# Optimization experiments

Measured on AMD Instinct MI355X. Metric: run time of the kernel, lower is better.

The kernel has to match this reference:

```python
import jax, jax.numpy as jnp
import numpy as np

H = 128          # hidden_size
GRID = 4         # grid_dim
CELL = 0.5       # cell_size
PRED_LEN = 12
EMB = H // 4     # social pooling embed dim = 32


def setup_inputs() -> dict:
    key = jax.random.key(0)
    ks = jax.random.split(key, 13)
    B, N, T = 16384, 64, 8
    s = 0.05
    return {
        "obs": jax.random.normal(ks[0], (B, T, 2), jnp.float32),
        "neighbors": jax.random.normal(ks[1], (B, N, T, 2), jnp.float32),
        "embed_table": jax.random.normal(ks[2], (GRID * GRID + 1, EMB), jnp.float32) * s,
        "W_in": jax.random.normal(ks[3], (H, 2), jnp.float32) * s,
        "b_in": jax.random.normal(ks[4], (H,), jnp.float32) * s,
        "W_sp": jax.random.normal(ks[5], (H, EMB), jnp.float32) * s,
        "b_sp": jax.random.normal(ks[6], (H,), jnp.float32) * s,
        "W_ih": jax.random.normal(ks[7], (4 * H, 2 * H), jnp.float32) * s,
        "W_hh": jax.random.normal(ks[8], (4 * H, H), jnp.float32) * s,
        "b_ih": jax.random.normal(ks[9], (4 * H,), jnp.float32) * s,
        "b_hh": jax.random.normal(ks[10], (4 * H,), jnp.float32) * s,
        "W_out": jax.random.normal(ks[11], (2, H), jnp.float32) * s,
        "b_out": jax.random.normal(ks[12], (2,), jnp.float32) * s,
    }


def reference(obs, neighbors, embed_table, W_in, b_in, W_sp, b_sp,
              W_ih, W_hh, b_ih, b_hh, W_out, b_out):
    B = obs.shape[0]
    half = GRID // 2

    def pool(rel):  # rel: [B, N, 2] -> [B, EMB]
        idx = jnp.clip(jnp.floor(rel / CELL).astype(jnp.int32), -half, half - 1) + half
        # after clamp+shift, idx in [0, GRID-1], so index is always valid (matches torch path)
        flat = idx[..., 0] * GRID + idx[..., 1]  # [B, N]
        return embed_table[flat].sum(axis=1)     # sum-pool over neighbors

    def lstm(h, c, x):  # torch LSTMCell gate order: i, f, g, o
        gates = x @ W_ih.T + b_ih + h @ W_hh.T + b_hh  # [B, 4H]
        i, f, g, o = jnp.split(gates, 4, axis=-1)
        c2 = jax.nn.sigmoid(f) * c + jax.nn.sigmoid(i) * jnp.tanh(g)
        h2 = jax.nn.sigmoid(o) * jnp.tanh(c2)
        return h2, c2

    def obs_step(carry, xs):
        h, c = carry
        o_t, nb_t = xs  # [B,2], [B,N,2]
        agent = o_t @ W_in.T + b_in                        # [B,H]
        social = pool(nb_t - o_t[:, None, :]) @ W_sp.T + b_sp  # [B,H]
        h, c = lstm(h, c, jnp.concatenate([agent, social], axis=-1))
        return (h, c), None

    h0 = jnp.zeros((B, H), obs.dtype)
    c0 = jnp.zeros((B, H), obs.dtype)
    obs_tf = jnp.swapaxes(obs, 0, 1)          # [T,B,2]
    nb_tf = jnp.moveaxis(neighbors, 2, 0)     # [T,B,N,2]
    (h, c), _ = jax.lax.scan(obs_step, (h0, c0), (obs_tf, nb_tf))

    def pred_step(carry, _):
        h, c, prev = carry
        agent = prev @ W_in.T + b_in
        x = jnp.concatenate([agent, jnp.zeros_like(agent)], axis=-1)
        h, c = lstm(h, c, x)
        disp = h @ W_out.T + b_out  # [B,2]
        return (h, c, disp), disp

    prev0 = jnp.zeros((B, 2), obs.dtype)
    _, fut = jax.lax.scan(pred_step, (h, c, prev0), None, length=PRED_LEN)
    return jnp.swapaxes(fut, 0, 1)  # [B, PRED_LEN, 2]
```

## Files before the change

kernel.cpp:

```cpp
#include <hip/hip_runtime.h>
#include <math.h>

typedef _Float16 f16;
typedef f16 f16x8 __attribute__((ext_vector_type(8)));
typedef float f32x4 __attribute__((ext_vector_type(4)));

#define Bsz   16384
#define Tobs  8
#define PREDL 12
#define MR    32

__device__ __forceinline__ float fast_sigm(float x) {
  float e = __builtin_amdgcn_exp2f(-1.44269504f * x);
  return __builtin_amdgcn_rcpf(1.f + e);
}
__device__ __forceinline__ float fast_tanh(float x) {
  float e = __builtin_amdgcn_exp2f(2.88539008f * x);
  return 1.f - 2.f * __builtin_amdgcn_rcpf(1.f + e);
}


#define HB(buf, ct, kt, lane, j) (((((buf)*2 + (ct))*4 + (kt))*64 + (lane))*8 + (j))
#define CX(t, ct, lane, j) ((((t)*2 + (ct))*64 + (lane))*8 + (j))
#define WF(ktw, w, rt, lane) ((size_t)((((ktw)*16 + (w))*2 + (rt))*64 + (lane)) * 8)

__global__ __launch_bounds__(64) void pack_all(
    const float* __restrict__ W_ih, const float* __restrict__ W_hh,
    const float* __restrict__ W_in, const float* __restrict__ W_sp,
    const float* __restrict__ table,
    const float* __restrict__ b_in, const float* __restrict__ b_sp,
    const float* __restrict__ b_ih, const float* __restrict__ b_hh,
    const float* __restrict__ W_out, const float* __restrict__ b_out,
    f16* __restrict__ Wfrag, float* __restrict__ biasO,
    float* __restrict__ biasP, float* __restrict__ biasPE) {
  const int jo = blockIdx.x;
  const int g = jo >> 7, hc = jo & 127;
  const int w = hc >> 3, rt = (hc >> 2) & 1, qq = hc & 3;
  const int rowr = qq * 4 + g;
  const int m = threadIdx.x;
  __shared__ float wspPS[32];
  __shared__ float cellsS[16];

  float a0 = W_ih[jo * 256 + m],        a1 = W_ih[jo * 256 + 64 + m];
  float s0 = W_ih[jo * 256 + 128 + m],  s1 = W_ih[jo * 256 + 192 + m];
  float hh0 = W_hh[jo * 128 + m],       hh1 = W_hh[jo * 128 + 64 + m];
  float bi0 = b_in[m], bi1 = b_in[64 + m];
  float bs0 = b_sp[m], bs1 = b_sp[64 + m];
  float wi00 = W_in[m * 2 + 0],        wi01 = W_in[m * 2 + 1];
  float wi10 = W_in[(64 + m) * 2 + 0], wi11 = W_in[(64 + m) * 2 + 1];

  auto red = [](float v) {
#pragma unroll
    for (int s = 1; s < 64; s <<= 1) v += __shfl_xor(v, s);
    return v;
  };

#pragma unroll 4
  for (int e = 0; e < 32; ++e) {
    float wp = red(s0 * W_sp[m * 32 + e] + s1 * W_sp[(64 + m) * 32 + e]);
    if (m == e) wspPS[e] = wp;
  }
  __syncthreads();
  if (m < 16) {
    float s = 0.f;
#pragma unroll
    for (int e = 0; e < 32; ++e) s += table[m * 32 + e] * wspPS[e];
    cellsS[m] = s;
  }

  float wio0 = red(a0 * wi00 + a1 * wi10);
  float wio1 = red(a0 * wi01 + a1 * wi11);
  float dotA = red(a0 * bi0 + a1 * bi1);
  float dotS = red(s0 * bs0 + s1 * bs1);

  float eff0 = hh0 + wio0 * W_out[m]      + wio1 * W_out[128 + m];
  float eff1 = hh1 + wio0 * W_out[64 + m] + wio1 * W_out[192 + m];

  const int lane_w = ((m >> 3) & 3) * 16 + rowr;
  const int j_w = m & 7, kh = m >> 5;
  Wfrag[WF(kh,     w, rt, lane_w) + j_w] = (f16)hh0;
  Wfrag[WF(2 + kh, w, rt, lane_w) + j_w] = (f16)hh1;
  Wfrag[WF(5 + kh, w, rt, lane_w) + j_w] = (f16)eff0;
  Wfrag[WF(7 + kh, w, rt, lane_w) + j_w] = (f16)eff1;

  if (m < 32) {
    float x = (m < 16) ? cellsS[m] : (m == 16 ? wio0 : (m == 17 ? wio1 : 0.f));
    Wfrag[WF(4, w, rt, (m >> 3) * 16 + rowr) + (m & 7)] = (f16)x;
  }
  if (m == 36) {
    const int idx = ((w * 2 + rt) * 4 + qq) * 4 + g;
    const float base = b_ih[jo] + b_hh[jo];
    biasO[idx] = base + dotA + dotS;
    biasP[idx] = base + dotA;
    biasPE[idx] = base + dotA + wio0 * b_out[0] + wio1 * b_out[1];
  }
}

__global__ __launch_bounds__(1024, 4) void social_lstm_main(
    const float* __restrict__ obs, const float* __restrict__ nb,
    const f16* __restrict__ Wfrag, const float* __restrict__ biasO,
    const float* __restrict__ biasP, const float* __restrict__ biasPE,
    const float* __restrict__ W_out, const float* __restrict__ b_out,
    float* __restrict__ out) {
  __shared__ __align__(16) f16 Hbuf[2 * 2 * 4 * 64 * 8];
  __shared__ __align__(16) f16 cntX[8 * 2 * 64 * 8];

  const int tid = threadIdx.x;
  const int w = tid >> 6, ln = tid & 63;
  const int q = ln >> 4, c = ln & 15;
  const int b0 = blockIdx.x * MR;

  for (int i = tid; i < 2048; i += 1024) ((uint32_t*)Hbuf)[i] = 0u;
  for (int i = tid; i < 8192; i += 1024) ((uint32_t*)cntX)[i] = 0u;
  __syncthreads();

  {
    const int r = tid >> 5;
    const int lg = tid & 31;
    const float4* orow = (const float4*)(obs + (size_t)(b0 + r) * 16);
    float4 O0 = orow[0], O1 = orow[1], O2 = orow[2], O3 = orow[3];
    float ox[8] = {O0.x, O0.z, O1.x, O1.z, O2.x, O2.z, O3.x, O3.z};
    float oy[8] = {O0.y, O0.w, O1.y, O1.w, O2.y, O2.w, O3.y, O3.w};
    unsigned long long h[8] = {0ull, 0ull, 0ull, 0ull, 0ull, 0ull, 0ull, 0ull};
#pragma unroll
    for (int jt = 0; jt < 2; ++jt) {
      int trk = lg + 32 * jt;
      const float4* tr = (const float4*)(nb + ((size_t)(b0 + r) * 64 + trk) * 16);
      float4 T0 = tr[0], T1 = tr[1], T2 = tr[2], T3 = tr[3];
      float nx[8] = {T0.x, T0.z, T1.x, T1.z, T2.x, T2.z, T3.x, T3.z};
      float ny[8] = {T0.y, T0.w, T1.y, T1.w, T2.y, T2.w, T3.y, T3.w};
#pragma unroll
      for (int t = 0; t < 8; ++t) {
        float rx = nx[t] - ox[t], ry = ny[t] - oy[t];
        int ix = (int)floorf(rx + rx);
        int iy = (int)floorf(ry + ry);
        ix = min(max(ix, -2), 1);
        iy = min(max(iy, -2), 1);
        int flat = (ix + 2) * 4 + (iy + 2);
        h[t] += 1ull << (flat * 4);
      }
    }
    auto shx = [](unsigned long long x, int msk) {
      unsigned lo = __shfl_xor((unsigned)x, msk);
      unsigned hi = __shfl_xor((unsigned)(x >> 32), msk);
      return ((unsigned long long)hi << 32) | lo;
    };
#pragma unroll
    for (int t = 0; t < 8; ++t) {
      unsigned long long e0 = h[t] & 0x0F0F0F0F0F0F0F0Full;
      unsigned long long e1 = (h[t] >> 4) & 0x0F0F0F0F0F0F0F0Full;
      e0 += shx(e0, 1);  e1 += shx(e1, 1);
      e0 += shx(e0, 2);  e1 += shx(e1, 2);
      e0 += shx(e0, 4);  e1 += shx(e1, 4);
      e0 += shx(e0, 8);  e1 += shx(e1, 8);
      e0 += shx(e0, 16); e1 += shx(e1, 16);
      if (lg < 16) {
        unsigned long long src = (lg & 1) ? e1 : e0;
        unsigned cnt = (unsigned)(src >> ((lg >> 1) * 8)) & 0xFFu;
        cntX[CX(t, r >> 4, (lg >> 3) * 16 + (r & 15), lg & 7)] = (f16)(float)cnt;
      }
    }
    if (lg < 8) {
      float xv = obs[(size_t)(b0 + r) * 16 + lg * 2];
      float yv = obs[(size_t)(b0 + r) * 16 + lg * 2 + 1];
      cntX[CX(lg, r >> 4, 2 * 16 + (r & 15), 0)] = (f16)xv;
      cntX[CX(lg, r >> 4, 2 * 16 + (r & 15), 1)] = (f16)yv;
    }
  }

  f16x8 Wh[2][4];
#pragma unroll
  for (int rt = 0; rt < 2; ++rt)
#pragma unroll
    for (int kt = 0; kt < 4; ++kt)
      Wh[rt][kt] = *(const f16x8*)(Wfrag + WF(kt, w, rt, ln));

  float creg[4] = {0.f, 0.f, 0.f, 0.f};
  const int ktw_i = w >> 2;
  const int lnw = (w & 3) * 16 + c;
  const int bi0i = (w * 2 + 0) * 4 + q, bi1i = (w * 2 + 1) * 4 + q;

  auto epi = [&](f32x4 a, int rt, int ct, int wb) {
    float iv = fast_sigm(a[0]), fv = fast_sigm(a[1]);
    float gv = fast_tanh(a[2]), ov = fast_sigm(a[3]);
    int ci = rt * 2 + ct;
    float c2 = fv * creg[ci] + iv * gv;
    creg[ci] = c2;
    float hv = ov * fast_tanh(c2);
    Hbuf[HB(wb, ct, ktw_i, lnw, rt * 4 + q)] = (f16)hv;
  };

  auto hh_chain = [&](int rb, f32x4& a00, f32x4& a01, f32x4& a10, f32x4& a11) {
#pragma unroll
    for (int kt = 0; kt < 4; ++kt) {
      f16x8 h0 = *(const f16x8*)&Hbuf[HB(rb, 0, kt, ln, 0)];
      f16x8 h1 = *(const f16x8*)&Hbuf[HB(rb, 1, kt, ln, 0)];
      a00 = __builtin_amdgcn_mfma_f32_16x16x32_f16(Wh[0][kt], h0, a00, 0, 0, 0);
      a01 = __builtin_amdgcn_mfma_f32_16x16x32_f16(Wh[0][kt], h1, a01, 0, 0, 0);
      a10 = __builtin_amdgcn_mfma_f32_16x16x32_f16(Wh[1][kt], h0, a10, 0, 0, 0);
      a11 = __builtin_amdgcn_mfma_f32_16x16x32_f16(Wh[1][kt], h1, a11, 0, 0, 0);
    }
  };

  {
    f16x8 Bx0 = *(const f16x8*)(Wfrag + WF(4, w, 0, ln));
    f16x8 Bx1 = *(const f16x8*)(Wfrag + WF(4, w, 1, ln));
#pragma unroll
    for (int t = 0; t < Tobs; ++t) {
      const int rb = t & 1, wb = rb ^ 1;
      __syncthreads();
      float4 bv0 = ((const float4*)biasO)[bi0i];
      float4 bv1 = ((const float4*)biasO)[bi1i];
      f32x4 a00 = (f32x4){bv0.x, bv0.y, bv0.z, bv0.w}, a01 = a00;
      f32x4 a10 = (f32x4){bv1.x, bv1.y, bv1.z, bv1.w}, a11 = a10;
      f16x8 c0 = *(const f16x8*)&cntX[CX(t, 0, ln, 0)];
      f16x8 c1 = *(const f16x8*)&cntX[CX(t, 1, ln, 0)];
      a00 = __builtin_amdgcn_mfma_f32_16x16x32_f16(Bx0, c0, a00, 0, 0, 0);
      a01 = __builtin_amdgcn_mfma_f32_16x16x32_f16(Bx0, c1, a01, 0, 0, 0);
      a10 = __builtin_amdgcn_mfma_f32_16x16x32_f16(Bx1, c0, a10, 0, 0, 0);
      a11 = __builtin_amdgcn_mfma_f32_16x16x32_f16(Bx1, c1, a11, 0, 0, 0);
      hh_chain(rb, a00, a01, a10, a11);
      epi(a00, 0, 0, wb); epi(a01, 0, 1, wb);
      epi(a10, 1, 0, wb); epi(a11, 1, 1, wb);
    }
  }

  {
    const int rb = Tobs & 1, wb = rb ^ 1;
    __syncthreads();
    float4 bv0 = ((const float4*)biasP)[bi0i];
    float4 bv1 = ((const float4*)biasP)[bi1i];
    f32x4 a00 = (f32x4){bv0.x, bv0.y, bv0.z, bv0.w}, a01 = a00;
    f32x4 a10 = (f32x4){bv1.x, bv1.y, bv1.z, bv1.w}, a11 = a10;
    hh_chain(rb, a00, a01, a10, a11);
    epi(a00, 0, 0, wb); epi(a01, 0, 1, wb);
    epi(a10, 1, 0, wb); epi(a11, 1, 1, wb);
  }

#pragma unroll
  for (int rt = 0; rt < 2; ++rt)
#pragma unroll
    for (int kt = 0; kt < 4; ++kt)
      Wh[rt][kt] = *(const f16x8*)(Wfrag + WF(5 + kt, w, rt, ln));

  const int d_oi = tid >> 4, d_s = tid & 15;
  const int d_row = d_oi >> 1, d_jj = d_oi & 1;
  const float d_bo = b_out[d_jj];

  auto disp_out = [&](int rbuf, int p) {
    const float4* wp = (const float4*)(W_out + d_jj * 128 + d_s * 8);
    float4 w0 = wp[0], w1 = wp[1];
    f16x8 h8 = *(const f16x8*)&Hbuf[
        HB(rbuf, d_row >> 4, d_s >> 2, (d_s & 3) * 16 + (d_row & 15), 0)];
    float s = w0.x * (float)h8[0] + w0.y * (float)h8[1] +
              w0.z * (float)h8[2] + w0.w * (float)h8[3] +
              w1.x * (float)h8[4] + w1.y * (float)h8[5] +
              w1.z * (float)h8[6] + w1.w * (float)h8[7];
    s += __shfl_xor(s, 1);
    s += __shfl_xor(s, 2);
    s += __shfl_xor(s, 4);
    s += __shfl_xor(s, 8);
    if ((tid & 15) == 0)
      out[(size_t)(b0 + d_row) * (PREDL * 2) + p * 2 + d_jj] = s + d_bo;
  };

  for (int p = 1; p < PREDL; ++p) {
    const int st = Tobs + p;
    const int rb = st & 1, wb = rb ^ 1;
    __syncthreads();
    disp_out(rb, p - 1);
    float4 bv0 = ((const float4*)biasPE)[bi0i];
    float4 bv1 = ((const float4*)biasPE)[bi1i];
    f32x4 a00 = (f32x4){bv0.x, bv0.y, bv0.z, bv0.w}, a01 = a00;
    f32x4 a10 = (f32x4){bv1.x, bv1.y, bv1.z, bv1.w}, a11 = a10;
    hh_chain(rb, a00, a01, a10, a11);
    epi(a00, 0, 0, wb); epi(a01, 0, 1, wb);
    epi(a10, 1, 0, wb); epi(a11, 1, 1, wb);
  }
  __syncthreads();
  disp_out((Tobs + PREDL) & 1, PREDL - 1);
}

extern "C" void kernel_launch(void* const* d_in, const int* in_sizes, int n_in,
                              void* d_out, int out_size, void* d_ws, size_t ws_size,
                              hipStream_t stream) {
  const float* obs   = (const float*)d_in[0];
  const float* nbrs  = (const float*)d_in[1];
  const float* table = (const float*)d_in[2];
  const float* W_in  = (const float*)d_in[3];
  const float* b_in  = (const float*)d_in[4];
  const float* W_sp  = (const float*)d_in[5];
  const float* b_sp  = (const float*)d_in[6];
  const float* W_ih  = (const float*)d_in[7];
  const float* W_hh  = (const float*)d_in[8];
  const float* b_ih  = (const float*)d_in[9];
  const float* b_hh  = (const float*)d_in[10];
  const float* W_out = (const float*)d_in[11];
  const float* b_out = (const float*)d_in[12];
  float* out = (float*)d_out;

  char* ws = (char*)d_ws;
  f16*   Wfrag  = (f16*)(ws);
  float* biasO  = (float*)(ws + 294912);
  float* biasP  = (float*)(ws + 296960);
  float* biasPE = (float*)(ws + 299008);

  pack_all<<<512, 64, 0, stream>>>(W_ih, W_hh, W_in, W_sp, table, b_in, b_sp, b_ih, b_hh,
                                   W_out, b_out, Wfrag, biasO, biasP, biasPE);
  social_lstm_main<<<Bsz / MR, 1024, 0, stream>>>(obs, nbrs, Wfrag, biasO, biasP, biasPE,
                                                  W_out, b_out, out);
}
```

Baseline: 210.9 us.

## Process two 32-row groups per block with interleaved MFMA chains and packed h stores

Measured after the change: 205.1 us. 2.8% less time.

```diff
diff --git a/kernel.cpp b/kernel.cpp
--- a/kernel.cpp
+++ b/kernel.cpp
@@ -2,13 +2,14 @@
 #include <math.h>
 
 typedef _Float16 f16;
+typedef f16 f16x2 __attribute__((ext_vector_type(2)));
 typedef f16 f16x8 __attribute__((ext_vector_type(8)));
 typedef float f32x4 __attribute__((ext_vector_type(4)));
 
 #define Bsz   16384
 #define Tobs  8
 #define PREDL 12
-#define MR    32
+#define MR    64
 
 __device__ __forceinline__ float fast_sigm(float x) {
   float e = __builtin_amdgcn_exp2f(-1.44269504f * x);
@@ -20,8 +21,6 @@
 }
 
 
-#define HB(buf, ct, kt, lane, j) (((((buf)*2 + (ct))*4 + (kt))*64 + (lane))*8 + (j))
-#define CX(t, ct, lane, j) ((((t)*2 + (ct))*64 + (lane))*8 + (j))
 #define WF(ktw, w, rt, lane) ((size_t)((((ktw)*16 + (w))*2 + (rt))*64 + (lane)) * 8)
 
 __global__ __launch_bounds__(64) void pack_all(
@@ -32,7 +31,8 @@
     const float* __restrict__ b_ih, const float* __restrict__ b_hh,
     const float* __restrict__ W_out, const float* __restrict__ b_out,
     f16* __restrict__ Wfrag, float* __restrict__ biasO,
-    float* __restrict__ biasP, float* __restrict__ biasPE) {
+    float* __restrict__ biasP, float* __restrict__ biasPE,
+    float* __restrict__ W_outP) {
   const int jo = blockIdx.x;
   const int g = jo >> 7, hc = jo & 127;
   const int w = hc >> 3, rt = (hc >> 2) & 1, qq = hc & 3;
@@ -76,8 +76,9 @@
   float eff0 = hh0 + wio0 * W_out[m]      + wio1 * W_out[128 + m];
   float eff1 = hh1 + wio0 * W_out[64 + m] + wio1 * W_out[192 + m];
 
-  const int lane_w = ((m >> 3) & 3) * 16 + rowr;
-  const int j_w = m & 7, kh = m >> 5;
+  const int km = (m & 0x78) | (2 * (m & 3) + ((m >> 2) & 1));
+  const int lane_w = ((km >> 3) & 3) * 16 + rowr;
+  const int j_w = km & 7, kh = km >> 5;
   Wfrag[WF(kh,     w, rt, lane_w) + j_w] = (f16)hh0;
   Wfrag[WF(2 + kh, w, rt, lane_w) + j_w] = (f16)hh1;
   Wfrag[WF(5 + kh, w, rt, lane_w) + j_w] = (f16)eff0;
@@ -94,37 +95,47 @@
     biasP[idx] = base + dotA;
     biasPE[idx] = base + dotA + wio0 * b_out[0] + wio1 * b_out[1];
   }
-}
-
-__global__ __launch_bounds__(1024, 4) void social_lstm_main(
+  if (jo == 0) {
+    W_outP[km]            = W_out[m];
+    W_outP[km + 64]       = W_out[m + 64];
+    W_outP[128 + km]      = W_out[128 + m];
+    W_outP[128 + km + 64] = W_out[128 + m + 64];
+  }
+}
+
+__global__ __launch_bounds__(1024) void social_lstm_main(
     const float* __restrict__ obs, const float* __restrict__ nb,
     const f16* __restrict__ Wfrag, const float* __restrict__ biasO,
     const float* __restrict__ biasP, const float* __restrict__ biasPE,
-    const float* __restrict__ W_out, const float* __restrict__ b_out,
+    const float* __restrict__ W_outP, const float* __restrict__ b_out,
     float* __restrict__ out) {
-  __shared__ __align__(16) f16 Hbuf[2 * 2 * 4 * 64 * 8];
-  __shared__ __align__(16) f16 cntX[8 * 2 * 64 * 8];
+  __shared__ __align__(16) f16 Hbuf[2][2][2][4][64][8];
+  __shared__ __align__(16) f16 cntX[2][8][2][64][8];
 
   const int tid = threadIdx.x;
   const int w = tid >> 6, ln = tid & 63;
   const int q = ln >> 4, c = ln & 15;
+  const int whi = w >> 2, wlo = w & 3;
   const int b0 = blockIdx.x * MR;
 
-  for (int i = tid; i < 2048; i += 1024) ((uint32_t*)Hbuf)[i] = 0u;
-  for (int i = tid; i < 8192; i += 1024) ((uint32_t*)cntX)[i] = 0u;
+  for (int i = tid; i < 16384; i += 1024) {
+    ((uint32_t*)Hbuf)[i] = 0u;
+    ((uint32_t*)cntX)[i] = 0u;
+  }
   __syncthreads();
 
   {
-    const int r = tid >> 5;
-    const int lg = tid & 31;
+    const int r = tid >> 4;
+    const int lg = tid & 15;
+    const int pG = r >> 5, prr = r & 31;
     const float4* orow = (const float4*)(obs + (size_t)(b0 + r) * 16);
     float4 O0 = orow[0], O1 = orow[1], O2 = orow[2], O3 = orow[3];
     float ox[8] = {O0.x, O0.z, O1.x, O1.z, O2.x, O2.z, O3.x, O3.z};
     float oy[8] = {O0.y, O0.w, O1.y, O1.w, O2.y, O2.w, O3.y, O3.w};
     unsigned long long h[8] = {0ull, 0ull, 0ull, 0ull, 0ull, 0ull, 0ull, 0ull};
 #pragma unroll
-    for (int jt = 0; jt < 2; ++jt) {
-      int trk = lg + 32 * jt;
+    for (int jt = 0; jt < 4; ++jt) {
+      int trk = lg + 16 * jt;
       const float4* tr = (const float4*)(nb + ((size_t)(b0 + r) * 64 + trk) * 16);
       float4 T0 = tr[0], T1 = tr[1], T2 = tr[2], T3 = tr[3];
       float nx[8] = {T0.x, T0.z, T1.x, T1.z, T2.x, T2.z, T3.x, T3.z};
@@ -149,22 +160,19 @@
     for (int t = 0; t < 8; ++t) {
       unsigned long long e0 = h[t] & 0x0F0F0F0F0F0F0F0Full;
       unsigned long long e1 = (h[t] >> 4) & 0x0F0F0F0F0F0F0F0Full;
-      e0 += shx(e0, 1);  e1 += shx(e1, 1);
-      e0 += shx(e0, 2);  e1 += shx(e1, 2);
-      e0 += shx(e0, 4);  e1 += shx(e1, 4);
-      e0 += shx(e0, 8);  e1 += shx(e1, 8);
-      e0 += shx(e0, 16); e1 += shx(e1, 16);
-      if (lg < 16) {
-        unsigned long long src = (lg & 1) ? e1 : e0;
-        unsigned cnt = (unsigned)(src >> ((lg >> 1) * 8)) & 0xFFu;
-        cntX[CX(t, r >> 4, (lg >> 3) * 16 + (r & 15), lg & 7)] = (f16)(float)cnt;
-      }
+      e0 += shx(e0, 1); e1 += shx(e1, 1);
+      e0 += shx(e0, 2); e1 += shx(e1, 2);
+      e0 += shx(e0, 4); e1 += shx(e1, 4);
+      e0 += shx(e0, 8); e1 += shx(e1, 8);
+      unsigned long long src = (lg & 1) ? e1 : e0;
+      unsigned cnt = (unsigned)(src >> ((lg >> 1) * 8)) & 0xFFu;
+      cntX[pG][t][prr >> 4][(lg >> 3) * 16 + (prr & 15)][lg & 7] = (f16)(float)cnt;
     }
     if (lg < 8) {
       float xv = obs[(size_t)(b0 + r) * 16 + lg * 2];
       float yv = obs[(size_t)(b0 + r) * 16 + lg * 2 + 1];
-      cntX[CX(lg, r >> 4, 2 * 16 + (r & 15), 0)] = (f16)xv;
-      cntX[CX(lg, r >> 4, 2 * 16 + (r & 15), 1)] = (f16)yv;
+      cntX[pG][lg][prr >> 4][2 * 16 + (prr & 15)][0] = (f16)xv;
+      cntX[pG][lg][prr >> 4][2 * 16 + (prr & 15)][1] = (f16)yv;
     }
   }
 
@@ -175,107 +183,124 @@
     for (int kt = 0; kt < 4; ++kt)
       Wh[rt][kt] = *(const f16x8*)(Wfrag + WF(kt, w, rt, ln));
 
-  float creg[4] = {0.f, 0.f, 0.f, 0.f};
-  const int ktw_i = w >> 2;
-  const int lnw = (w & 3) * 16 + c;
-  const int bi0i = (w * 2 + 0) * 4 + q, bi1i = (w * 2 + 1) * 4 + q;
-
-  auto epi = [&](f32x4 a, int rt, int ct, int wb) {
+  float cr[8];
+#pragma unroll
+  for (int i = 0; i < 8; ++i) cr[i] = 0.f;
+
+  auto ldbias = [&](const float* bp, f32x4& v0, f32x4& v1) {
+    float4 t0 = ((const float4*)bp)[(w * 2 + 0) * 4 + q];
+    float4 t1 = ((const float4*)bp)[(w * 2 + 1) * 4 + q];
+    v0 = (f32x4){t0.x, t0.y, t0.z, t0.w};
+    v1 = (f32x4){t1.x, t1.y, t1.z, t1.w};
+  };
+
+  auto mf = [](f16x8 a, f16x8 b, f32x4 cc) {
+    return __builtin_amdgcn_mfma_f32_16x16x32_f16(a, b, cc, 0, 0, 0);
+  };
+
+  auto cell = [&](const f32x4& a, float& ccst) {
     float iv = fast_sigm(a[0]), fv = fast_sigm(a[1]);
     float gv = fast_tanh(a[2]), ov = fast_sigm(a[3]);
-    int ci = rt * 2 + ct;
-    float c2 = fv * creg[ci] + iv * gv;
-    creg[ci] = c2;
-    float hv = ov * fast_tanh(c2);
-    Hbuf[HB(wb, ct, ktw_i, lnw, rt * 4 + q)] = (f16)hv;
-  };
-
-  auto hh_chain = [&](int rb, f32x4& a00, f32x4& a01, f32x4& a10, f32x4& a11) {
+    ccst = fv * ccst + iv * gv;
+    return ov * fast_tanh(ccst);
+  };
+
+  f16x8 Bx0 = *(const f16x8*)(Wfrag + WF(4, w, 0, ln));
+  f16x8 Bx1 = *(const f16x8*)(Wfrag + WF(4, w, 1, ln));
+
+  f32x4 bv0, bv1;
+  ldbias(biasO, bv0, bv1);
+
+  auto step = [&](int rb, int wb, bool ex, int t) {
+    f32x4 A00 = bv0, A01 = bv0, A10 = bv1, A11 = bv1;
+    f32x4 B00 = bv0, B01 = bv0, B10 = bv1, B11 = bv1;
+    if (ex) {
+      f16x8 ca0 = *(const f16x8*)&cntX[0][t][0][ln][0];
+      f16x8 ca1 = *(const f16x8*)&cntX[0][t][1][ln][0];
+      A00 = mf(Bx0, ca0, A00); A01 = mf(Bx0, ca1, A01);
+      A10 = mf(Bx1, ca0, A10); A11 = mf(Bx1, ca1, A11);
+      f16x8 cb0 = *(const f16x8*)&cntX[1][t][0][ln][0];
+      f16x8 cb1 = *(const f16x8*)&cntX[1][t][1][ln][0];
+      B00 = mf(Bx0, cb0, B00); B01 = mf(Bx0, cb1, B01);
+      B10 = mf(Bx1, cb0, B10); B11 = mf(Bx1, cb1, B11);
+    }
 #pragma unroll
     for (int kt = 0; kt < 4; ++kt) {
-      f16x8 h0 = *(const f16x8*)&Hbuf[HB(rb, 0, kt, ln, 0)];
-      f16x8 h1 = *(const f16x8*)&Hbuf[HB(rb, 1, kt, ln, 0)];
-      a00 = __builtin_amdgcn_mfma_f32_16x16x32_f16(Wh[0][kt], h0, a00, 0, 0, 0);
-      a01 = __builtin_amdgcn_mfma_f32_16x16x32_f16(Wh[0][kt], h1, a01, 0, 0, 0);
-      a10 = __builtin_amdgcn_mfma_f32_16x16x32_f16(Wh[1][kt], h0, a10, 0, 0, 0);
-      a11 = __builtin_amdgcn_mfma_f32_16x16x32_f16(Wh[1][kt], h1, a11, 0, 0, 0);
-    }
-  };
-
-  {
-    f16x8 Bx0 = *(const f16x8*)(Wfrag + WF(4, w, 0, ln));
-    f16x8 Bx1 = *(const f16x8*)(Wfrag + WF(4, w, 1, ln));
-#pragma unroll
-    for (int t = 0; t < Tobs; ++t) {
-      const int rb = t & 1, wb = rb ^ 1;
-      __syncthreads();
-      float4 bv0 = ((const float4*)biasO)[bi0i];
-      float4 bv1 = ((const float4*)biasO)[bi1i];
-      f32x4 a00 = (f32x4){bv0.x, bv0.y, bv0.z, bv0.w}, a01 = a00;
-      f32x4 a10 = (f32x4){bv1.x, bv1.y, bv1.z, bv1.w}, a11 = a10;
-      f16x8 c0 = *(const f16x8*)&cntX[CX(t, 0, ln, 0)];
-      f16x8 c1 = *(const f16x8*)&cntX[CX(t, 1, ln, 0)];
-      a00 = __builtin_amdgcn_mfma_f32_16x16x32_f16(Bx0, c0, a00, 0, 0, 0);
-      a01 = __builtin_amdgcn_mfma_f32_16x16x32_f16(Bx0, c1, a01, 0, 0, 0);
-      a10 = __builtin_amdgcn_mfma_f32_16x16x32_f16(Bx1, c0, a10, 0, 0, 0);
-      a11 = __builtin_amdgcn_mfma_f32_16x16x32_f16(Bx1, c1, a11, 0, 0, 0);
-      hh_chain(rb, a00, a01, a10, a11);
-      epi(a00, 0, 0, wb); epi(a01, 0, 1, wb);
-      epi(a10, 1, 0, wb); epi(a11, 1, 1, wb);
-    }
-  }
-
-  {
-    const int rb = Tobs & 1, wb = rb ^ 1;
+      f16x8 h0 = *(const f16x8*)&Hbuf[0][rb][0][kt][ln][0];
+      f16x8 h1 = *(const f16x8*)&Hbuf[0][rb][1][kt][ln][0];
+      A00 = mf(Wh[0][kt], h0, A00); A01 = mf(Wh[0][kt], h1, A01);
+      A10 = mf(Wh[1][kt], h0, A10); A11 = mf(Wh[1][kt], h1, A11);
+    }
+#pragma unroll
+    for (int kt = 0; kt < 4; ++kt) {
+      f16x8 h0 = *(const f16x8*)&Hbuf[1][rb][0][kt][ln][0];
+      f16x8 h1 = *(const f16x8*)&Hbuf[1][rb][1][kt][ln][0];
+      B00 = mf(Wh[0][kt], h0, B00); B01 = mf(Wh[0][kt], h1, B01);
+      B10 = mf(Wh[1][kt], h0, B10); B11 = mf(Wh[1][kt], h1, B11);
+    }
+    {
+      f16x2 pk;
+      pk[0] = (f16)cell(A00, cr[0]); pk[1] = (f16)cell(A10, cr[2]);
+      *(f16x2*)&Hbuf[0][wb][0][whi][wlo * 16 + c][2 * q] = pk;
+      pk[0] = (f16)cell(A01, cr[1]); pk[1] = (f16)cell(A11, cr[3]);
+      *(f16x2*)&Hbuf[0][wb][1][whi][wlo * 16 + c][2 * q] = pk;
+      pk[0] = (f16)cell(B00, cr[4]); pk[1] = (f16)cell(B10, cr[6]);
+      *(f16x2*)&Hbuf[1][wb][0][whi][wlo * 16 + c][2 * q] = pk;
+      pk[0] = (f16)cell(B01, cr[5]); pk[1] = (f16)cell(B11, cr[7]);
+      *(f16x2*)&Hbuf[1][wb][1][whi][wlo * 16 + c][2 * q] = pk;
+    }
+  };
+
+#pragma unroll
+  for (int t = 0; t < Tobs; ++t) {
+    const int rb = t & 1;
     __syncthreads();
-    float4 bv0 = ((const float4*)biasP)[bi0i];
-    float4 bv1 = ((const float4*)biasP)[bi1i];
-    f32x4 a00 = (f32x4){bv0.x, bv0.y, bv0.z, bv0.w}, a01 = a00;
-    f32x4 a10 = (f32x4){bv1.x, bv1.y, bv1.z, bv1.w}, a11 = a10;
-    hh_chain(rb, a00, a01, a10, a11);
-    epi(a00, 0, 0, wb); epi(a01, 0, 1, wb);
-    epi(a10, 1, 0, wb); epi(a11, 1, 1, wb);
-  }
+    step(rb, rb ^ 1, true, t);
+  }
+
+  ldbias(biasP, bv0, bv1);
+  __syncthreads();
+  step(0, 1, false, 0);
 
 #pragma unroll
   for (int rt = 0; rt < 2; ++rt)
 #pragma unroll
     for (int kt = 0; kt < 4; ++kt)
       Wh[rt][kt] = *(const f16x8*)(Wfrag + WF(5 + kt, w, rt, ln));
-
-  const int d_oi = tid >> 4, d_s = tid & 15;
+  ldbias(biasPE, bv0, bv1);
+
+  const int d_oi = tid >> 3, d_s8 = tid & 7;
   const int d_row = d_oi >> 1, d_jj = d_oi & 1;
+  const int dG = d_row >> 5, drr = d_row & 31;
+  const int d_ct = drr >> 4, d_c = drr & 15;
+  const int d_kt = d_s8 >> 1, d_fl = (2 * (d_s8 & 1)) * 16 + d_c;
   const float d_bo = b_out[d_jj];
 
   auto disp_out = [&](int rbuf, int p) {
-    const float4* wp = (const float4*)(W_out + d_jj * 128 + d_s * 8);
-    float4 w0 = wp[0], w1 = wp[1];
-    f16x8 h8 = *(const f16x8*)&Hbuf[
-        HB(rbuf, d_row >> 4, d_s >> 2, (d_s & 3) * 16 + (d_row & 15), 0)];
-    float s = w0.x * (float)h8[0] + w0.y * (float)h8[1] +
-              w0.z * (float)h8[2] + w0.w * (float)h8[3] +
-              w1.x * (float)h8[4] + w1.y * (float)h8[5] +
-              w1.z * (float)h8[6] + w1.w * (float)h8[7];
+    const float4* wp = (const float4*)(W_outP + d_jj * 128 + d_s8 * 16);
+    float4 w0 = wp[0], w1 = wp[1], w2 = wp[2], w3 = wp[3];
+    f16x8 e0 = *(const f16x8*)&Hbuf[dG][rbuf][d_ct][d_kt][d_fl][0];
+    f16x8 e1 = *(const f16x8*)&Hbuf[dG][rbuf][d_ct][d_kt][d_fl + 16][0];
+    float s = w0.x * (float)e0[0] + w0.y * (float)e0[1] +
+              w0.z * (float)e0[2] + w0.w * (float)e0[3] +
+              w1.x * (float)e0[4] + w1.y * (float)e0[5] +
+              w1.z * (float)e0[6] + w1.w * (float)e0[7] +
+              w2.x * (float)e1[0] + w2.y * (float)e1[1] +
+              w2.z * (float)e1[2] + w2.w * (float)e1[3] +
+              w3.x * (float)e1[4] + w3.y * (float)e1[5] +
+              w3.z * (float)e1[6] + w3.w * (float)e1[7];
     s += __shfl_xor(s, 1);
     s += __shfl_xor(s, 2);
     s += __shfl_xor(s, 4);
-    s += __shfl_xor(s, 8);
-    if ((tid & 15) == 0)
+    if ((tid & 7) == 0)
       out[(size_t)(b0 + d_row) * (PREDL * 2) + p * 2 + d_jj] = s + d_bo;
   };
 
   for (int p = 1; p < PREDL; ++p) {
-    const int st = Tobs + p;
-    const int rb = st & 1, wb = rb ^ 1;
+    const int rb = p & 1;
     __syncthreads();
     disp_out(rb, p - 1);
-    float4 bv0 = ((const float4*)biasPE)[bi0i];
-    float4 bv1 = ((const float4*)biasPE)[bi1i];
-    f32x4 a00 = (f32x4){bv0.x, bv0.y, bv0.z, bv0.w}, a01 = a00;
-    f32x4 a10 = (f32x4){bv1.x, bv1.y, bv1.z, bv1.w}, a11 = a10;
-    hh_chain(rb, a00, a01, a10, a11);
-    epi(a00, 0, 0, wb); epi(a01, 0, 1, wb);
-    epi(a10, 1, 0, wb); epi(a11, 1, 1, wb);
+    step(rb, rb ^ 1, false, 0);
   }
   __syncthreads();
   disp_out((Tobs + PREDL) & 1, PREDL - 1);
@@ -304,9 +329,10 @@
   float* biasO  = (float*)(ws + 294912);
   float* biasP  = (float*)(ws + 296960);
   float* biasPE = (float*)(ws + 299008);
+  float* W_outP = (float*)(ws + 301056);
 
   pack_all<<<512, 64, 0, stream>>>(W_ih, W_hh, W_in, W_sp, table, b_in, b_sp, b_ih, b_hh,
-                                   W_out, b_out, Wfrag, biasO, biasP, biasPE);
+                                   W_out, b_out, Wfrag, biasO, biasP, biasPE, W_outP);
   social_lstm_main<<<Bsz / MR, 1024, 0, stream>>>(obs, nbrs, Wfrag, biasO, biasP, biasPE,
-                                                  W_out, b_out, out);
-}
+                                                  W_outP, b_out, out);
+}
```
